# Kernel tuning notes

Hardware: AMD Instinct MI355X
Metric: run time of the kernel (lower is better)

The kernel has to match this reference:

```python
import jax, jax.numpy as jnp
import numpy as np

B, BITS, HID = 4096, 64, 512
EPS = 1e-5
TEMPERATURE = 1.0  # buffer default


def _w(k, shape):
    return jax.random.normal(k, shape, jnp.float32) * 0.02


def setup_inputs() -> dict:
    key = jax.random.key(0)
    ks = jax.random.split(key, 8)
    return {
        "a_bits": jax.random.uniform(ks[0], (B, BITS), jnp.float32),
        "shift_bits": jax.random.uniform(ks[1], (B, BITS), jnp.float32),
        # shift_decoder params
        "W1": _w(ks[2], (HID, BITS)), "b1": jnp.zeros((HID,), jnp.float32),
        "g1": jnp.ones((HID,), jnp.float32), "be1": jnp.zeros((HID,), jnp.float32),
        "W2": _w(ks[3], (HID, HID)), "b2": jnp.zeros((HID,), jnp.float32),
        "g2": jnp.ones((HID,), jnp.float32), "be2": jnp.zeros((HID,), jnp.float32),
        "W3": _w(ks[4], (BITS, HID)), "b3": jnp.zeros((BITS,), jnp.float32),
        # index_net params (input dim = 2*BITS)
        "Wi1": _w(ks[5], (HID, 2 * BITS)), "bi1": jnp.zeros((HID,), jnp.float32),
        "Wi2": _w(ks[6], (HID, HID)), "bi2": jnp.zeros((HID,), jnp.float32),
        "Wi3": _w(ks[7], (BITS, HID)), "bi3": jnp.zeros((BITS,), jnp.float32),
    }


def _layernorm(x, g, b):
    m = jnp.mean(x, axis=-1, keepdims=True)
    v = jnp.mean(jnp.square(x - m), axis=-1, keepdims=True)
    return (x - m) * jax.lax.rsqrt(v + EPS) * g + b


def reference(a_bits, shift_bits, W1, b1, g1, be1, W2, b2, g2, be2, W3, b3,
              Wi1, bi1, Wi2, bi2, Wi3, bi3):
    # shift decoder: Linear -> LN -> ReLU -> Linear -> LN -> ReLU -> Linear
    h = jax.nn.relu(_layernorm(shift_bits @ W1.T + b1, g1, be1))
    h = jax.nn.relu(_layernorm(h @ W2.T + b2, g2, be2))
    shift_logits = h @ W3.T + b3                        # [B, BITS]
    shift_soft = jax.nn.softmax(shift_logits / TEMPERATURE, axis=-1)

    # index_net, vectorized over the output-position loop.
    # combined = [one_hot(i), shift_soft]; the one-hot part of the first Linear
    # just selects column i of Wi1[:, :BITS], so we add it as a [BITS, HID] bias.
    pos_part = Wi1[:, :BITS].T                          # [BITS, HID]
    shift_part = shift_soft @ Wi1[:, BITS:].T           # [B, HID]
    h1 = jax.nn.relu(pos_part[None, :, :] + shift_part[:, None, :] + bi1)  # [B, BITS, HID]
    h2 = jax.nn.relu(jnp.einsum('bph,kh->bpk', h1, Wi2) + bi2)             # [B, BITS, HID]
    idx_logits = jnp.einsum('bph,kh->bpk', h2, Wi3) + bi3                  # [B, BITS, BITS]
    idx_soft = jax.nn.softmax(idx_logits / TEMPERATURE, axis=-1)

    # softmax-weighted gather-sum over a_bits
    return jnp.einsum('bpj,bj->bp', idx_soft, a_bits)   # [B, BITS]
```

## Files before the change

### kernel.cpp

```cpp
#include <hip/hip_runtime.h>
#include <hip/hip_bf16.h>
#include <math.h>

#define B_N 4096
#define BITSN 64
#define HID 512
#define EPSV 1e-5f
#define BT 16

typedef unsigned short ushort_t;
typedef __attribute__((ext_vector_type(8))) short bf16x8;
typedef __attribute__((ext_vector_type(4))) float f32x4;
typedef __attribute__((ext_vector_type(16))) float f32x16;

__device__ __forceinline__ ushort_t f2bf(float f) {
  unsigned u = __float_as_uint(f);
  u += 0x7FFF + ((u >> 16) & 1);
  return (ushort_t)(u >> 16);
}

__device__ __forceinline__ unsigned pack2bf(float lo, float hi) {
  union { __hip_bfloat162 h; unsigned u; } cv;
  cv.h = __float22bfloat162_rn(make_float2(lo, hi));
  return cv.u;
}

__global__ __launch_bounds__(256) void prep_kernel(
    const float* __restrict__ Wi2, const float* __restrict__ Wi3,
    const float* __restrict__ Wi1, const float* __restrict__ W1,
    const float* __restrict__ W2, const float* __restrict__ W3,
    float* __restrict__ Wi1posT, ushort_t* __restrict__ W1b,
    ushort_t* __restrict__ W2b, ushort_t* __restrict__ W3b,
    ushort_t* __restrict__ Wi1sb, ushort_t* __restrict__ Wi2f32,
    ushort_t* __restrict__ Wi3f) {
  int idx = blockIdx.x * 256 + threadIdx.x;
  if (idx < 512 * 512) {
    W2b[idx] = f2bf(W2[idx]);
    int j = idx & 7, lane = (idx >> 3) & 63;
    int ct = (idx >> 9) & 15, ks = idx >> 13;
    int c = ct * 32 + (lane & 31);
    int k = ks * 16 + (lane >> 5) * 8 + j;
    Wi2f32[idx] = f2bf(Wi2[c * 512 + k]);
  }
  if (idx < 64 * 512) {
    W3b[idx] = f2bf(W3[idx]);
    int p = idx >> 9, i = idx & 511;
    Wi1posT[idx] = Wi1[i * 128 + p];
    int j = idx & 7, lane = (idx >> 3) & 63;
    int nt = (idx >> 9) & 3, ks2 = idx >> 11;
    int jr = nt * 16 + (lane & 15);
    int k = ks2 * 32 + (lane >> 4) * 8 + j;
    Wi3f[idx] = f2bf(Wi3[jr * 512 + k]);
  }
  if (idx < 512 * 64) {
    W1b[idx] = f2bf(W1[idx]);
    int j = idx >> 6, k = idx & 63;
    Wi1sb[idx] = f2bf(Wi1[j * 128 + 64 + k]);
  }
}

__global__ __launch_bounds__(256) void shift2_kernel(
    const float* __restrict__ shift_bits,
    const ushort_t* __restrict__ W1b, const float* __restrict__ b1,
    const float* __restrict__ g1, const float* __restrict__ be1,
    const ushort_t* __restrict__ W2b, const float* __restrict__ b2,
    const float* __restrict__ g2, const float* __restrict__ be2,
    const ushort_t* __restrict__ W3b, const float* __restrict__ b3,
    const ushort_t* __restrict__ Wi1sb, const float* __restrict__ bi1,
    float* __restrict__ sp) {
  __shared__ __align__(16) ushort_t hA[BT * 512];
  __shared__ __align__(16) char reg2[32 * 1024];
  __shared__ float b1s[512], g1s[512], be1s[512];
  __shared__ float b2s[512], g2s[512], be2s[512], bi1s[512];
  __shared__ float red[4][BT][2];
  __shared__ float b3s[64];

  ushort_t* sbt = (ushort_t*)reg2;
  ushort_t* Bs  = (ushort_t*)reg2;
  ushort_t* h2  = (ushort_t*)reg2;
  float (*lg32)[68] = (float(*)[68])(reg2 + 16 * 1024);
  ushort_t* sb2 = (ushort_t*)(reg2 + 16 * 1024 + 16 * 68 * 4);

  int b0 = blockIdx.x * BT;
  int t = threadIdx.x, w = t >> 6, l = t & 63, lg = l >> 4, l15 = l & 15;

  b1s[t] = b1[t];  b1s[t + 256] = b1[t + 256];
  g1s[t] = g1[t];  g1s[t + 256] = g1[t + 256];
  be1s[t] = be1[t]; be1s[t + 256] = be1[t + 256];
  b2s[t] = b2[t];  b2s[t + 256] = b2[t + 256];
  g2s[t] = g2[t];  g2s[t + 256] = g2[t + 256];
  be2s[t] = be2[t]; be2s[t + 256] = be2[t + 256];
  bi1s[t] = bi1[t]; bi1s[t + 256] = bi1[t + 256];
  if (t < 64) b3s[t] = b3[t];
  if (t < 128) {
    int row = t >> 3, g = t & 7;
    const float* src = shift_bits + (size_t)(b0 + row) * 64 + g * 8;
    uint4 pk;
    pk.x = (unsigned)f2bf(src[0]) | ((unsigned)f2bf(src[1]) << 16);
    pk.y = (unsigned)f2bf(src[2]) | ((unsigned)f2bf(src[3]) << 16);
    pk.z = (unsigned)f2bf(src[4]) | ((unsigned)f2bf(src[5]) << 16);
    pk.w = (unsigned)f2bf(src[6]) | ((unsigned)f2bf(src[7]) << 16);
    *(uint4*)((char*)sbt + ((row * 128 + g * 16) ^ ((row & 7) << 4))) = pk;
  }
  __syncthreads();

  f32x4 acc[8];
#pragma unroll
  for (int nt = 0; nt < 8; ++nt) acc[nt] = (f32x4){0.f, 0.f, 0.f, 0.f};
#pragma unroll
  for (int ks = 0; ks < 2; ++ks) {
    bf16x8 af = *(const bf16x8*)((char*)sbt + ((l15 * 128 + ks * 64 + lg * 16) ^ ((l15 & 7) << 4)));
#pragma unroll
    for (int nt = 0; nt < 8; ++nt) {
      int c = w * 128 + nt * 16 + l15;
      bf16x8 bfr = *(const bf16x8*)(W1b + (size_t)c * 64 + ks * 32 + lg * 8);
      acc[nt] = __builtin_amdgcn_mfma_f32_16x16x32_bf16(af, bfr, acc[nt], 0, 0, 0);
    }
  }
  {
    float s[4] = {0.f, 0.f, 0.f, 0.f}, q[4] = {0.f, 0.f, 0.f, 0.f};
#pragma unroll
    for (int nt = 0; nt < 8; ++nt) {
      int c = w * 128 + nt * 16 + l15;
      float bb = b1s[c];
#pragma unroll
      for (int r = 0; r < 4; ++r) {
        float x = acc[nt][r] + bb;
        acc[nt][r] = x;
        s[r] += x; q[r] += x * x;
      }
    }
#pragma unroll
    for (int m = 8; m >= 1; m >>= 1)
#pragma unroll
      for (int r = 0; r < 4; ++r) { s[r] += __shfl_xor(s[r], m); q[r] += __shfl_xor(q[r], m); }
    if (l15 == 0)
#pragma unroll
      for (int r = 0; r < 4; ++r) { red[w][4 * lg + r][0] = s[r]; red[w][4 * lg + r][1] = q[r]; }
    __syncthreads();
    float mean[4], rs[4];
#pragma unroll
    for (int r = 0; r < 4; ++r) {
      int p = 4 * lg + r;
      float S = red[0][p][0] + red[1][p][0] + red[2][p][0] + red[3][p][0];
      float Q = red[0][p][1] + red[1][p][1] + red[2][p][1] + red[3][p][1];
      mean[r] = S * (1.0f / 512.0f);
      float var = Q * (1.0f / 512.0f) - mean[r] * mean[r];
      rs[r] = rsqrtf(var + EPSV);
    }
#pragma unroll
    for (int nt = 0; nt < 8; ++nt) {
      int c = w * 128 + nt * 16 + l15;
      float gg = g1s[c], bb = be1s[c];
#pragma unroll
      for (int r = 0; r < 4; ++r) {
        int p = 4 * lg + r;
        float v = (acc[nt][r] - mean[r]) * rs[r] * gg + bb;
        v = v > 0.f ? v : 0.f;
        *(ushort_t*)((char*)hA + ((p * 1024 + c * 2) ^ ((p & 7) << 4))) = f2bf(v);
      }
    }
  }
  __syncthreads();

#pragma unroll
  for (int nt = 0; nt < 8; ++nt) acc[nt] = (f32x4){0.f, 0.f, 0.f, 0.f};
  for (int step = 0; step < 16; ++step) {
    int i0 = step * 32;
#pragma unroll
    for (int qq = 0; qq < 8; ++qq) {
      int g = qq * 256 + t;
      int c = g >> 2, xg = g & 3;
      int ic = xg ^ ((c >> 1) & 3);
      ((uint4*)Bs)[g] = *(const uint4*)(W2b + (size_t)c * 512 + i0 + ic * 8);
    }
    __syncthreads();
    bf16x8 af = *(const bf16x8*)((char*)hA + ((l15 * 1024 + step * 64 + lg * 16) ^ ((l15 & 7) << 4)));
#pragma unroll
    for (int nt = 0; nt < 8; ++nt) {
      int c = w * 128 + nt * 16 + l15;
      bf16x8 bfr = ((const bf16x8*)Bs)[c * 4 + (lg ^ ((c >> 1) & 3))];
      acc[nt] = __builtin_amdgcn_mfma_f32_16x16x32_bf16(af, bfr, acc[nt], 0, 0, 0);
    }
    __syncthreads();
  }
  {
    float s[4] = {0.f, 0.f, 0.f, 0.f}, q[4] = {0.f, 0.f, 0.f, 0.f};
#pragma unroll
    for (int nt = 0; nt < 8; ++nt) {
      int c = w * 128 + nt * 16 + l15;
      float bb = b2s[c];
#pragma unroll
      for (int r = 0; r < 4; ++r) {
        float x = acc[nt][r] + bb;
        acc[nt][r] = x;
        s[r] += x; q[r] += x * x;
      }
    }
#pragma unroll
    for (int m = 8; m >= 1; m >>= 1)
#pragma unroll
      for (int r = 0; r < 4; ++r) { s[r] += __shfl_xor(s[r], m); q[r] += __shfl_xor(q[r], m); }
    if (l15 == 0)
#pragma unroll
      for (int r = 0; r < 4; ++r) { red[w][4 * lg + r][0] = s[r]; red[w][4 * lg + r][1] = q[r]; }
    __syncthreads();
    float mean[4], rs[4];
#pragma unroll
    for (int r = 0; r < 4; ++r) {
      int p = 4 * lg + r;
      float S = red[0][p][0] + red[1][p][0] + red[2][p][0] + red[3][p][0];
      float Q = red[0][p][1] + red[1][p][1] + red[2][p][1] + red[3][p][1];
      mean[r] = S * (1.0f / 512.0f);
      float var = Q * (1.0f / 512.0f) - mean[r] * mean[r];
      rs[r] = rsqrtf(var + EPSV);
    }
#pragma unroll
    for (int nt = 0; nt < 8; ++nt) {
      int c = w * 128 + nt * 16 + l15;
      float gg = g2s[c], bb = be2s[c];
#pragma unroll
      for (int r = 0; r < 4; ++r) {
        int p = 4 * lg + r;
        float v = (acc[nt][r] - mean[r]) * rs[r] * gg + bb;
        v = v > 0.f ? v : 0.f;
        *(ushort_t*)((char*)h2 + ((p * 1024 + c * 2) ^ ((p & 7) << 4))) = f2bf(v);
      }
    }
  }
  __syncthreads();

  {
    f32x4 a3 = (f32x4){0.f, 0.f, 0.f, 0.f};
#pragma unroll
    for (int ks = 0; ks < 16; ++ks) {
      bf16x8 af = *(const bf16x8*)((char*)h2 + ((l15 * 1024 + ks * 64 + lg * 16) ^ ((l15 & 7) << 4)));
      bf16x8 bfr = *(const bf16x8*)(W3b + (size_t)(w * 16 + l15) * 512 + ks * 32 + lg * 8);
      a3 = __builtin_amdgcn_mfma_f32_16x16x32_bf16(af, bfr, a3, 0, 0, 0);
    }
    int c = w * 16 + l15;
    float bb = b3s[c];
#pragma unroll
    for (int r = 0; r < 4; ++r) lg32[4 * lg + r][c] = a3[r] + bb;
  }
  __syncthreads();

  {
    int r = t >> 4, j = t & 15;
    float v[4];
    float m = -1e30f;
#pragma unroll
    for (int mq = 0; mq < 4; ++mq) { v[mq] = lg32[r][mq * 16 + j]; m = fmaxf(m, v[mq]); }
#pragma unroll
    for (int mk = 8; mk >= 1; mk >>= 1) m = fmaxf(m, __shfl_xor(m, mk));
    float ssum = 0.f;
#pragma unroll
    for (int mq = 0; mq < 4; ++mq) { v[mq] = expf(v[mq] - m); ssum += v[mq]; }
#pragma unroll
    for (int mk = 8; mk >= 1; mk >>= 1) ssum += __shfl_xor(ssum, mk);
    float inv = 1.f / ssum;
#pragma unroll
    for (int mq = 0; mq < 4; ++mq) {
      int c = mq * 16 + j;
      *(ushort_t*)((char*)sb2 + ((r * 128 + c * 2) ^ ((r & 7) << 4))) = f2bf(v[mq] * inv);
    }
  }
  __syncthreads();

  {
    f32x4 a4[8];
#pragma unroll
    for (int nt = 0; nt < 8; ++nt) a4[nt] = (f32x4){0.f, 0.f, 0.f, 0.f};
#pragma unroll
    for (int ks = 0; ks < 2; ++ks) {
      bf16x8 af = *(const bf16x8*)((char*)sb2 + ((l15 * 128 + ks * 64 + lg * 16) ^ ((l15 & 7) << 4)));
#pragma unroll
      for (int nt = 0; nt < 8; ++nt) {
        int c = w * 128 + nt * 16 + l15;
        bf16x8 bfr = *(const bf16x8*)(Wi1sb + (size_t)c * 64 + ks * 32 + lg * 8);
        a4[nt] = __builtin_amdgcn_mfma_f32_16x16x32_bf16(af, bfr, a4[nt], 0, 0, 0);
      }
    }
#pragma unroll
    for (int nt = 0; nt < 8; ++nt) {
      int c = w * 128 + nt * 16 + l15;
      float bb = bi1s[c];
#pragma unroll
      for (int r = 0; r < 4; ++r)
        sp[(size_t)(b0 + 4 * lg + r) * 512 + c] = a4[nt][r] + bb;
    }
  }
}

__global__ __launch_bounds__(512, 4) void big5_kernel(
    const float* __restrict__ a_bits, const float* __restrict__ sp,
    const float* __restrict__ Wi1posT,
    const ushort_t* __restrict__ Wi2f32, const ushort_t* __restrict__ Wi3f,
    const float* __restrict__ bi2, const float* __restrict__ bi3,
    float* __restrict__ out) {
  __shared__ __align__(16) ushort_t h1s[64 * 512];
  __shared__ float bi2s[512];
  __shared__ float ab[64];
  __shared__ float bi3s[64];

  int b = blockIdx.x, t = threadIdx.x;
  int w = t >> 6, l = t & 63, lg = l >> 4, l15 = l & 15;
  int l31 = l & 31, hi = l >> 5;

  bi2s[t] = bi2[t];
  if (t < 64) { ab[t] = a_bits[b * 64 + t]; bi3s[t] = bi3[t]; }

  {
    const float* sprow = sp + (size_t)b * 512 + l * 8;
    float4 s0 = *(const float4*)(sprow);
    float4 s1 = *(const float4*)(sprow + 4);
#pragma unroll
    for (int g = 0; g < 8; ++g) {
      int p = g * 8 + w;
      const float4* pr = (const float4*)(Wi1posT + (size_t)p * 512 + l * 8);
      float4 p0 = pr[0], p1 = pr[1];
      float v0 = fmaxf(s0.x + p0.x, 0.f), v1 = fmaxf(s0.y + p0.y, 0.f);
      float v2 = fmaxf(s0.z + p0.z, 0.f), v3 = fmaxf(s0.w + p0.w, 0.f);
      float v4 = fmaxf(s1.x + p1.x, 0.f), v5 = fmaxf(s1.y + p1.y, 0.f);
      float v6 = fmaxf(s1.z + p1.z, 0.f), v7 = fmaxf(s1.w + p1.w, 0.f);
      uint4 pk;
      pk.x = pack2bf(v0, v1); pk.y = pack2bf(v2, v3);
      pk.z = pack2bf(v4, v5); pk.w = pack2bf(v6, v7);
      *(uint4*)((char*)h1s + ((p * 1024 + l * 16) ^ ((p & 15) << 4))) = pk;
    }
  }
  __syncthreads();

  f32x16 acc[2][2];
#pragma unroll
  for (int mt = 0; mt < 2; ++mt)
#pragma unroll
    for (int nt = 0; nt < 2; ++nt)
#pragma unroll
      for (int r = 0; r < 16; ++r) acc[mt][nt][r] = 0.f;

  const bf16x8* bbase = (const bf16x8*)Wi2f32 + ((size_t)(2 * w) * 64 + l);
  bf16x8 bA[2], bB[2];
#pragma unroll
  for (int n = 0; n < 2; ++n) bA[n] = bbase[n * 64];

  for (int ks = 0; ks < 32; ks += 2) {
#pragma unroll
    for (int n = 0; n < 2; ++n) bB[n] = bbase[(size_t)(ks + 1) * 1024 + n * 64];
    {
      bf16x8 af[2];
#pragma unroll
      for (int mt = 0; mt < 2; ++mt) {
        int row = mt * 32 + l31;
        af[mt] = *(const bf16x8*)((char*)h1s + ((row * 1024 + ks * 32 + hi * 16) ^ ((row & 15) << 4)));
      }
#pragma unroll
      for (int mt = 0; mt < 2; ++mt)
#pragma unroll
        for (int nt = 0; nt < 2; ++nt)
          acc[mt][nt] = __builtin_amdgcn_mfma_f32_32x32x16_bf16(af[mt], bA[nt], acc[mt][nt], 0, 0, 0);
    }
    if (ks < 30) {
#pragma unroll
      for (int n = 0; n < 2; ++n) bA[n] = bbase[(size_t)(ks + 2) * 1024 + n * 64];
    }
    {
      bf16x8 af[2];
#pragma unroll
      for (int mt = 0; mt < 2; ++mt) {
        int row = mt * 32 + l31;
        af[mt] = *(const bf16x8*)((char*)h1s + ((row * 1024 + (ks + 1) * 32 + hi * 16) ^ ((row & 15) << 4)));
      }
#pragma unroll
      for (int mt = 0; mt < 2; ++mt)
#pragma unroll
        for (int nt = 0; nt < 2; ++nt)
          acc[mt][nt] = __builtin_amdgcn_mfma_f32_32x32x16_bf16(af[mt], bB[nt], acc[mt][nt], 0, 0, 0);
    }
  }
  __syncthreads();

#pragma unroll
  for (int mt = 0; mt < 2; ++mt) {
#pragma unroll
    for (int nt = 0; nt < 2; ++nt) {
      int c = w * 64 + nt * 32 + l31;
      float bi = bi2s[c];
#pragma unroll
      for (int r = 0; r < 16; ++r) {
        int row = mt * 32 + (r & 3) + 8 * (r >> 2) + 4 * hi;
        float v = acc[mt][nt][r] + bi;
        v = v > 0.f ? v : 0.f;
        *(ushort_t*)((char*)h1s + ((row * 1024 + c * 2) ^ ((row & 15) << 4))) = f2bf(v);
      }
    }
  }
  __syncthreads();

  if (w < 4) {
    f32x4 lacc[4];
#pragma unroll
    for (int n = 0; n < 4; ++n) lacc[n] = (f32x4){0.f, 0.f, 0.f, 0.f};
    int p2 = 16 * w + l15;
    const bf16x8* b3base = (const bf16x8*)Wi3f + l;
#pragma unroll 4
    for (int ks2 = 0; ks2 < 16; ++ks2) {
      bf16x8 a2 = *(const bf16x8*)((char*)h1s + ((p2 * 1024 + ks2 * 64 + lg * 16) ^ ((p2 & 15) << 4)));
#pragma unroll
      for (int nt2 = 0; nt2 < 4; ++nt2) {
        bf16x8 b2v = b3base[(ks2 * 4 + nt2) * 64];
        lacc[nt2] = __builtin_amdgcn_mfma_f32_16x16x32_bf16(a2, b2v, lacc[nt2], 0, 0, 0);
      }
    }

#pragma unroll
    for (int r = 0; r < 4; ++r) {
      float v[4];
      float m = -1e30f;
#pragma unroll
      for (int nt2 = 0; nt2 < 4; ++nt2) {
        v[nt2] = lacc[nt2][r] + bi3s[nt2 * 16 + l15];
        m = fmaxf(m, v[nt2]);
      }
#pragma unroll
      for (int mm = 8; mm >= 1; mm >>= 1) m = fmaxf(m, __shfl_xor(m, mm));
      float s = 0.f, g = 0.f;
#pragma unroll
      for (int nt2 = 0; nt2 < 4; ++nt2) {
        float e = expf(v[nt2] - m);
        s += e;
        g += e * ab[nt2 * 16 + l15];
      }
#pragma unroll
      for (int mm = 8; mm >= 1; mm >>= 1) { s += __shfl_xor(s, mm); g += __shfl_xor(g, mm); }
      if (l15 == 0) out[b * 64 + 16 * w + 4 * lg + r] = g / s;
    }
  }
}

extern "C" void kernel_launch(void* const* d_in, const int* in_sizes, int n_in,
                              void* d_out, int out_size, void* d_ws, size_t ws_size,
                              hipStream_t stream) {
  const float* a_bits     = (const float*)d_in[0];
  const float* shift_bits = (const float*)d_in[1];
  const float* W1  = (const float*)d_in[2];
  const float* b1  = (const float*)d_in[3];
  const float* g1  = (const float*)d_in[4];
  const float* be1 = (const float*)d_in[5];
  const float* W2  = (const float*)d_in[6];
  const float* b2  = (const float*)d_in[7];
  const float* g2  = (const float*)d_in[8];
  const float* be2 = (const float*)d_in[9];
  const float* W3  = (const float*)d_in[10];
  const float* b3  = (const float*)d_in[11];
  const float* Wi1 = (const float*)d_in[12];
  const float* bi1 = (const float*)d_in[13];
  const float* Wi2 = (const float*)d_in[14];
  const float* bi2 = (const float*)d_in[15];
  const float* Wi3 = (const float*)d_in[16];
  const float* bi3 = (const float*)d_in[17];
  float* out = (float*)d_out;

  float* sp = (float*)d_ws;
  ushort_t* W2b = (ushort_t*)((char*)d_ws + (size_t)B_N * HID * 4);
  ushort_t* W1b = W2b + 512 * 512;
  ushort_t* W3b = W1b + 512 * 64;
  ushort_t* Wi1sb = W3b + 64 * 512;
  float* Wi1posT = (float*)(Wi1sb + 512 * 64);
  ushort_t* Wi2f32 = (ushort_t*)(Wi1posT + 64 * 512);
  ushort_t* Wi3f = Wi2f32 + 512 * 512;

  prep_kernel<<<1024, 256, 0, stream>>>(Wi2, Wi3, Wi1, W1, W2, W3,
                                        Wi1posT, W1b, W2b, W3b, Wi1sb, Wi2f32, Wi3f);
  shift2_kernel<<<B_N / BT, 256, 0, stream>>>(shift_bits, W1b, b1, g1, be1,
                                              W2b, b2, g2, be2, W3b, b3, Wi1sb, bi1, sp);
  big5_kernel<<<B_N, 512, 0, stream>>>(a_bits, sp, Wi1posT, Wi2f32, Wi3f, bi2, bi3, out);
}
```

Measured before the change: 215.0 us.

## Swap MFMA operands to compute transposed tile, deepen weight prefetch, vectorize epilogue stores

The hidden-layer GEMM now passes the Wi2 weight fragment as the A operand and h1 activations as B, so each accumulator holds a transposed tile in which every lane owns four consecutive output columns. The epilogue then loads the bias as a float4 and writes four packed bf16 values per store instead of scalar ushort stores. Weight fragments are prefetched four k-steps ahead rather than one, to hide global-load latency. This raises register pressure (eight bf16x8 weight buffers in flight) under the 512x4 launch bound.

```diff
diff --git a/kernel.cpp b/kernel.cpp
--- a/kernel.cpp
+++ b/kernel.cpp
@@ -292,7 +292,7 @@
   }
 }
 
-__global__ __launch_bounds__(512, 4) void big5_kernel(
+__global__ __launch_bounds__(512, 4) void big6_kernel(
     const float* __restrict__ a_bits, const float* __restrict__ sp,
     const float* __restrict__ Wi1posT,
     const ushort_t* __restrict__ Wi2f32, const ushort_t* __restrict__ Wi3f,
@@ -333,65 +333,57 @@
 
   f32x16 acc[2][2];
 #pragma unroll
-  for (int mt = 0; mt < 2; ++mt)
-#pragma unroll
-    for (int nt = 0; nt < 2; ++nt)
-#pragma unroll
-      for (int r = 0; r < 16; ++r) acc[mt][nt][r] = 0.f;
+  for (int mc = 0; mc < 2; ++mc)
+#pragma unroll
+    for (int np = 0; np < 2; ++np)
+#pragma unroll
+      for (int r = 0; r < 16; ++r) acc[mc][np][r] = 0.f;
 
   const bf16x8* bbase = (const bf16x8*)Wi2f32 + ((size_t)(2 * w) * 64 + l);
-  bf16x8 bA[2], bB[2];
-#pragma unroll
-  for (int n = 0; n < 2; ++n) bA[n] = bbase[n * 64];
-
-  for (int ks = 0; ks < 32; ks += 2) {
-#pragma unroll
-    for (int n = 0; n < 2; ++n) bB[n] = bbase[(size_t)(ks + 1) * 1024 + n * 64];
-    {
-      bf16x8 af[2];
-#pragma unroll
-      for (int mt = 0; mt < 2; ++mt) {
-        int row = mt * 32 + l31;
-        af[mt] = *(const bf16x8*)((char*)h1s + ((row * 1024 + ks * 32 + hi * 16) ^ ((row & 15) << 4)));
-      }
-#pragma unroll
-      for (int mt = 0; mt < 2; ++mt)
-#pragma unroll
-        for (int nt = 0; nt < 2; ++nt)
-          acc[mt][nt] = __builtin_amdgcn_mfma_f32_32x32x16_bf16(af[mt], bA[nt], acc[mt][nt], 0, 0, 0);
-    }
-    if (ks < 30) {
-#pragma unroll
-      for (int n = 0; n < 2; ++n) bA[n] = bbase[(size_t)(ks + 2) * 1024 + n * 64];
-    }
-    {
-      bf16x8 af[2];
-#pragma unroll
-      for (int mt = 0; mt < 2; ++mt) {
-        int row = mt * 32 + l31;
-        af[mt] = *(const bf16x8*)((char*)h1s + ((row * 1024 + (ks + 1) * 32 + hi * 16) ^ ((row & 15) << 4)));
-      }
-#pragma unroll
-      for (int mt = 0; mt < 2; ++mt)
-#pragma unroll
-        for (int nt = 0; nt < 2; ++nt)
-          acc[mt][nt] = __builtin_amdgcn_mfma_f32_32x32x16_bf16(af[mt], bB[nt], acc[mt][nt], 0, 0, 0);
-    }
-  }
-  __syncthreads();
-
-#pragma unroll
-  for (int mt = 0; mt < 2; ++mt) {
-#pragma unroll
-    for (int nt = 0; nt < 2; ++nt) {
-      int c = w * 64 + nt * 32 + l31;
-      float bi = bi2s[c];
-#pragma unroll
-      for (int r = 0; r < 16; ++r) {
-        int row = mt * 32 + (r & 3) + 8 * (r >> 2) + 4 * hi;
-        float v = acc[mt][nt][r] + bi;
-        v = v > 0.f ? v : 0.f;
-        *(ushort_t*)((char*)h1s + ((row * 1024 + c * 2) ^ ((row & 15) << 4))) = f2bf(v);
+  bf16x8 wf[4][2];
+#pragma unroll
+  for (int d = 0; d < 4; ++d) {
+    wf[d][0] = bbase[(size_t)d * 1024];
+    wf[d][1] = bbase[(size_t)d * 1024 + 64];
+  }
+
+  for (int kb = 0; kb < 8; ++kb) {
+#pragma unroll
+    for (int d = 0; d < 4; ++d) {
+      int ks = kb * 4 + d;
+      bf16x8 w0 = wf[d][0], w1 = wf[d][1];
+      if (kb < 7) {
+        wf[d][0] = bbase[(size_t)(ks + 4) * 1024];
+        wf[d][1] = bbase[(size_t)(ks + 4) * 1024 + 64];
+      }
+      int row0 = l31, row1 = 32 + l31;
+      bf16x8 h0 = *(const bf16x8*)((char*)h1s + ((row0 * 1024 + ks * 32 + hi * 16) ^ ((row0 & 15) << 4)));
+      bf16x8 h1v = *(const bf16x8*)((char*)h1s + ((row1 * 1024 + ks * 32 + hi * 16) ^ ((row1 & 15) << 4)));
+      acc[0][0] = __builtin_amdgcn_mfma_f32_32x32x16_bf16(w0, h0, acc[0][0], 0, 0, 0);
+      acc[0][1] = __builtin_amdgcn_mfma_f32_32x32x16_bf16(w0, h1v, acc[0][1], 0, 0, 0);
+      acc[1][0] = __builtin_amdgcn_mfma_f32_32x32x16_bf16(w1, h0, acc[1][0], 0, 0, 0);
+      acc[1][1] = __builtin_amdgcn_mfma_f32_32x32x16_bf16(w1, h1v, acc[1][1], 0, 0, 0);
+    }
+  }
+  __syncthreads();
+
+#pragma unroll
+  for (int mc = 0; mc < 2; ++mc) {
+#pragma unroll
+    for (int np = 0; np < 2; ++np) {
+      int p = np * 32 + l31;
+#pragma unroll
+      for (int rq = 0; rq < 4; ++rq) {
+        int c0 = w * 64 + mc * 32 + 8 * rq + 4 * hi;
+        float4 bi4 = *(const float4*)(bi2s + c0);
+        float v0 = fmaxf(acc[mc][np][4 * rq + 0] + bi4.x, 0.f);
+        float v1 = fmaxf(acc[mc][np][4 * rq + 1] + bi4.y, 0.f);
+        float v2 = fmaxf(acc[mc][np][4 * rq + 2] + bi4.z, 0.f);
+        float v3 = fmaxf(acc[mc][np][4 * rq + 3] + bi4.w, 0.f);
+        uint2 pk;
+        pk.x = pack2bf(v0, v1);
+        pk.y = pack2bf(v2, v3);
+        *(uint2*)((char*)h1s + ((p * 1024 + c0 * 2) ^ ((p & 15) << 4))) = pk;
       }
     }
   }
@@ -474,5 +466,5 @@
                                         Wi1posT, W1b, W2b, W3b, Wi1sb, Wi2f32, Wi3f);
   shift2_kernel<<<B_N / BT, 256, 0, stream>>>(shift_bits, W1b, b1, g1, be1,
                                               W2b, b2, g2, be2, W3b, b3, Wi1sb, bi1, sp);
-  big5_kernel<<<B_N, 512, 0, stream>>>(a_bits, sp, Wi1posT, Wi2f32, Wi3f, bi2, bi3, out);
-}
+  big6_kernel<<<B_N, 512, 0, stream>>>(a_bits, sp, Wi1posT, Wi2f32, Wi3f, bi2, bi3, out);
+}
```

Result: no change. 213.1 us (-0.8%).
